# Optimization experiments

Measured on AMD Instinct MI355X. Metric: run time of the kernel, lower is better.

## Reference

```python
import jax, jax.numpy as jnp
import numpy as np


def setup_inputs() -> dict:
    key = jax.random.key(0)
    k1, k2, k3, k4 = jax.random.split(key, 4)
    L, d, n_tokens = 4096, 2048, 4096
    x = jax.random.normal(k1, (L, d), dtype=jnp.float32)
    Wq_w = jax.random.normal(k2, (d, d), dtype=jnp.float32) * (1.0 / np.sqrt(d))
    Pk = jax.random.normal(k3, (1, n_tokens, d), dtype=jnp.float32)
    Pv = jax.random.normal(k4, (1, n_tokens, d), dtype=jnp.float32)
    return {"x": x, "Wq_w": Wq_w, "Pk": Pk, "Pv": Pv, "sliding_window_size": 1024}


def reference(x, Wq_w, Pk, Pv, sliding_window_size):
    # x: (L, d); Pk/Pv: (1, n_tokens, d). Single-head cross attention to a
    # fixed parameter token bank with a bidirectional sliding-window mask
    # |q_idx - kv_idx| < sliding_window_size (flex_attention semantics,
    # default scale = 1/sqrt(d)).
    L, d = x.shape
    n_tokens = Pk.shape[1]
    scale = 1.0 / np.sqrt(d).astype(np.float32)

    q = x @ Wq_w.T                                    # (L, d)
    scores = jnp.einsum('ld,td->lt', q, Pk[0]) * scale  # (L, n_tokens)

    q_idx = jnp.arange(L)[:, None]
    kv_idx = jnp.arange(n_tokens)[None, :]
    mask = jnp.abs(q_idx - kv_idx) < sliding_window_size  # (L, n_tokens)

    neg_inf = jnp.asarray(jnp.finfo(scores.dtype).min, scores.dtype)
    probs = jax.nn.softmax(jnp.where(mask, scores, neg_inf), axis=-1)
    y = jnp.einsum('lt,td->ld', probs, Pv[0])         # (L, d)
    return y[None, :, :]                              # (1, L, d) after squeeze(1)
```

## Files before the change

### kernel.cpp

```cpp
#include <hip/hip_runtime.h>


using bf16x8 = __attribute__((ext_vector_type(8))) short;
using f32x4  = __attribute__((ext_vector_type(4))) float;

#define LDIM 4096
#define TDIM 4096
#define DDIM 2048

static __device__ __forceinline__ unsigned short f2bf(float f) {
  union { float f; unsigned u; } c; c.f = f;
  unsigned r = c.u + 0x7FFFu + ((c.u >> 16) & 1u);
  return (unsigned short)(r >> 16);
}
static __device__ __forceinline__ unsigned pack2(float a, float b) {
  return (unsigned)f2bf(a) | ((unsigned)f2bf(b) << 16);
}

static __device__ __forceinline__ void gload16(const void* g, void* l) {
  __builtin_amdgcn_global_load_lds((const __attribute__((address_space(1))) void*)g,
                                   (__attribute__((address_space(3))) void*)l, 16, 0, 0);
}

__global__ __launch_bounds__(256) void k_cvt(const float* __restrict__ in,
                                             unsigned short* __restrict__ out, int n8) {
  int i = blockIdx.x * 256 + threadIdx.x;
  if (i >= n8) return;
  const float4* p = (const float4*)(in + (size_t)i * 8);
  float4 a = p[0], b = p[1];
  uint4 o = { pack2(a.x, a.y), pack2(a.z, a.w), pack2(b.x, b.y), pack2(b.z, b.w) };
  *(uint4*)(out + (size_t)i * 8) = o;
}

__global__ __launch_bounds__(256) void k_trans(const float* __restrict__ V,
                                               unsigned short* __restrict__ Vt) {
  __shared__ unsigned short tile[64][65];
  const int t0 = blockIdx.x * 64;
  const int j0 = blockIdx.y * 64;
  const int tid = threadIdx.x;
  const int r = tid >> 4;
  const int c = (tid & 15) * 4;
#pragma unroll
  for (int rr = 0; rr < 64; rr += 16) {
    float4 v = *(const float4*)(V + (size_t)(t0 + r + rr) * DDIM + j0 + c);
    tile[r + rr][c + 0] = f2bf(v.x);
    tile[r + rr][c + 1] = f2bf(v.y);
    tile[r + rr][c + 2] = f2bf(v.z);
    tile[r + rr][c + 3] = f2bf(v.w);
  }
  __syncthreads();
#pragma unroll
  for (int rr = 0; rr < 64; rr += 16) {
    ushort4 o = { tile[c + 0][r + rr], tile[c + 1][r + rr],
                  tile[c + 2][r + rr], tile[c + 3][r + rr] };
    *(ushort4*)(Vt + (size_t)(j0 + r + rr) * TDIM + t0 + c) = o;
  }
}

static __device__ __forceinline__ void gemm_loop(const unsigned short* __restrict__ A,
                                                 const unsigned short* __restrict__ B,
                                                 int m0, int n0, long lda, long ldb,
                                                 int kbeg, int kend,
                                                 unsigned short* As, unsigned short* Bs,
                                                 f32x4 (&acc)[4][4]) {
  const int tid = threadIdx.x;
  const int wave = tid >> 6, lane = tid & 63;
  const int quad = lane >> 4, l16 = lane & 15;
  const int wm = wave >> 1, wn = wave & 1;
  const int srow = wave * 32 + (lane >> 2);
  const int scol = (lane & 3) * 8;

  for (int k0 = kbeg; k0 < kend; k0 += 32) {
    const unsigned short* gA = A + (long)(m0 + srow) * lda + k0 + scol;
    const unsigned short* gB = B + (long)(n0 + srow) * ldb + k0 + scol;
    gload16(gA,            As + wave * 1024);
    gload16(gA + 16 * lda, As + wave * 1024 + 512);
    gload16(gB,            Bs + wave * 1024);
    gload16(gB + 16 * ldb, Bs + wave * 1024 + 512);
    __syncthreads();
    bf16x8 af[4], bf[4];
#pragma unroll
    for (int i = 0; i < 4; i++)
      af[i] = *(const bf16x8*)&As[(wm * 64 + i * 16 + l16) * 32 + quad * 8];
#pragma unroll
    for (int i = 0; i < 4; i++)
      bf[i] = *(const bf16x8*)&Bs[(wn * 64 + i * 16 + l16) * 32 + quad * 8];
#pragma unroll
    for (int i = 0; i < 4; i++)
#pragma unroll
      for (int j = 0; j < 4; j++)
        acc[i][j] = __builtin_amdgcn_mfma_f32_16x16x32_bf16(af[i], bf[j], acc[i][j], 0, 0, 0);
    __syncthreads();
  }
}

__global__ __launch_bounds__(256) void k1_qgemm(const unsigned short* __restrict__ X,
                                                const unsigned short* __restrict__ W,
                                                unsigned short* __restrict__ q) {
  __shared__ __align__(16) unsigned short As[128 * 32];
  __shared__ __align__(16) unsigned short Bs[128 * 32];
  f32x4 acc[4][4] = {};
  const int m0 = blockIdx.y * 128, n0 = blockIdx.x * 128;
  gemm_loop(X, W, m0, n0, DDIM, DDIM, 0, DDIM, As, Bs, acc);
  const int tid = threadIdx.x;
  const int wave = tid >> 6, lane = tid & 63;
  const int quad = lane >> 4, l16 = lane & 15, wm = wave >> 1, wn = wave & 1;
#pragma unroll
  for (int i = 0; i < 4; i++)
#pragma unroll
    for (int j = 0; j < 4; j++)
#pragma unroll
      for (int r = 0; r < 4; r++) {
        int row = m0 + wm * 64 + i * 16 + quad * 4 + r;
        int col = n0 + wn * 64 + j * 16 + l16;
        q[(long)row * DDIM + col] = f2bf(acc[i][j][r]);
      }
}

__global__ __launch_bounds__(256) void k2_qk(const unsigned short* __restrict__ Q,
                                             const unsigned short* __restrict__ Kb,
                                             unsigned short* __restrict__ P,
                                             float* __restrict__ rowsum,
                                             const int* __restrict__ wptr) {
  const int w = *wptr;
  const int l0 = blockIdx.y * 128, t0 = blockIdx.x * 128;
  int lo = l0 - w + 1; if (lo < 0) lo = 0;
  int hi = l0 + 127 + w - 1; if (hi > TDIM - 1) hi = TDIM - 1;
  if ((int)blockIdx.x < (lo >> 7) || (int)blockIdx.x > (hi >> 7)) return;
  __shared__ __align__(16) unsigned short As[128 * 32];
  __shared__ __align__(16) unsigned short Bs[128 * 32];
  f32x4 acc[4][4] = {};
  gemm_loop(Q, Kb, l0, t0, DDIM, DDIM, 0, DDIM, As, Bs, acc);
  const float scale = 0.022097086912079608f;
  const int tid = threadIdx.x;
  const int wave = tid >> 6, lane = tid & 63;
  const int quad = lane >> 4, l16 = lane & 15, wm = wave >> 1, wn = wave & 1;
#pragma unroll
  for (int i = 0; i < 4; i++) {
    float rs[4] = {0.f, 0.f, 0.f, 0.f};
#pragma unroll
    for (int j = 0; j < 4; j++)
#pragma unroll
      for (int r = 0; r < 4; r++) {
        int l = l0 + wm * 64 + i * 16 + quad * 4 + r;
        int t = t0 + wn * 64 + j * 16 + l16;
        int dlt = l - t; dlt = dlt < 0 ? -dlt : dlt;
        float e = 0.f;
        if (dlt < w) e = __expf(acc[i][j][r] * scale);
        unsigned short bv = f2bf(e);
        P[(long)l * TDIM + t] = bv;
        rs[r] += __uint_as_float((unsigned)bv << 16);
      }
#pragma unroll
    for (int r = 0; r < 4; ++r) {
      float s = rs[r];
      s += __shfl_xor(s, 1);
      s += __shfl_xor(s, 2);
      s += __shfl_xor(s, 4);
      s += __shfl_xor(s, 8);
      if (l16 == 0) atomicAdd(&rowsum[l0 + wm * 64 + i * 16 + quad * 4 + r], s);
    }
  }
}

__global__ __launch_bounds__(256) void k3_pv(const unsigned short* __restrict__ P,
                                             const unsigned short* __restrict__ Vt,
                                             const float* __restrict__ rowsum,
                                             float* __restrict__ Y,
                                             const int* __restrict__ wptr) {
  const int w = *wptr;
  const int l0 = blockIdx.y * 128, j0 = blockIdx.x * 128;
  int lo = l0 - w + 1; if (lo < 0) lo = 0;
  int hi = l0 + 127 + w - 1; if (hi > TDIM - 1) hi = TDIM - 1;
  const int kb = (lo >> 7) * 128, ke = ((hi >> 7) + 1) * 128;
  __shared__ __align__(16) unsigned short As[128 * 32];
  __shared__ __align__(16) unsigned short Bs[128 * 32];
  f32x4 acc[4][4] = {};
  gemm_loop(P, Vt, l0, j0, TDIM, TDIM, kb, ke, As, Bs, acc);
  const int tid = threadIdx.x;
  const int wave = tid >> 6, lane = tid & 63;
  const int quad = lane >> 4, l16 = lane & 15, wm = wave >> 1, wn = wave & 1;
#pragma unroll
  for (int i = 0; i < 4; i++)
#pragma unroll
    for (int r = 0; r < 4; r++) {
      const int l = l0 + wm * 64 + i * 16 + quad * 4 + r;
      const float inv = 1.0f / rowsum[l];
#pragma unroll
      for (int j = 0; j < 4; j++)
        Y[(long)l * DDIM + j0 + wn * 64 + j * 16 + l16] = acc[i][j][r] * inv;
    }
}

extern "C" void kernel_launch(void* const* d_in, const int* in_sizes, int n_in,
                              void* d_out, int out_size, void* d_ws, size_t ws_size,
                              hipStream_t stream) {
  const float* x  = (const float*)d_in[0];
  const float* Wq = (const float*)d_in[1];
  const float* Pk = (const float*)d_in[2];
  const float* Pv = (const float*)d_in[3];
  const int* wptr = (const int*)d_in[4];
  float* Y = (float*)d_out;

  unsigned short* base = (unsigned short*)d_ws;
  unsigned short* Pm = base;
  unsigned short* xb = base;
  unsigned short* wb = base + (size_t)LDIM * DDIM;
  unsigned short* kb = base + (size_t)TDIM * TDIM;
  unsigned short* vt = kb + (size_t)TDIM * DDIM;
  unsigned short* qb = vt + (size_t)DDIM * TDIM;
  float* rowsum = (float*)(qb + (size_t)LDIM * DDIM);

  hipMemsetAsync(rowsum, 0, LDIM * sizeof(float), stream);
  k_cvt<<<LDIM * DDIM / 8 / 256, 256, 0, stream>>>(x, xb, LDIM * DDIM / 8);
  k_cvt<<<DDIM * DDIM / 8 / 256, 256, 0, stream>>>(Wq, wb, DDIM * DDIM / 8);
  k_cvt<<<TDIM * DDIM / 8 / 256, 256, 0, stream>>>(Pk, kb, TDIM * DDIM / 8);
  k_trans<<<dim3(TDIM / 64, DDIM / 64), 256, 0, stream>>>(Pv, vt);
  k1_qgemm<<<dim3(DDIM / 128, LDIM / 128), 256, 0, stream>>>(xb, wb, qb);
  k2_qk<<<dim3(TDIM / 128, LDIM / 128), 256, 0, stream>>>(qb, kb, Pm, rowsum, wptr);
  k3_pv<<<dim3(DDIM / 128, LDIM / 128), 256, 0, stream>>>(Pm, vt, rowsum, Y, wptr);
}
```

Measured before the change: 319.0 us.

## Fuse prep kernels and widen GEMM K-tile to 64 with XOR-swizzled LDS

Merges the three fp32-to-bf16 conversion launches, the V transpose and the rowsum memset into one prep kernel, removing several launches. The transpose now writes 16-byte vector stores. The shared GEMM loop moves from a K step of 32 to 64 and uses an XOR swizzle on LDS chunks, which halves the number of barriers per unit of K and is meant to cut LDS bank conflicts on fragment reads. This doubles the LDS footprint per block, which may reduce occupancy.

```diff
diff --git a/kernel.cpp b/kernel.cpp
--- a/kernel.cpp
+++ b/kernel.cpp
@@ -16,45 +16,55 @@
 static __device__ __forceinline__ unsigned pack2(float a, float b) {
   return (unsigned)f2bf(a) | ((unsigned)f2bf(b) << 16);
 }
-
 static __device__ __forceinline__ void gload16(const void* g, void* l) {
   __builtin_amdgcn_global_load_lds((const __attribute__((address_space(1))) void*)g,
                                    (__attribute__((address_space(3))) void*)l, 16, 0, 0);
 }
 
-__global__ __launch_bounds__(256) void k_cvt(const float* __restrict__ in,
-                                             unsigned short* __restrict__ out, int n8) {
-  int i = blockIdx.x * 256 + threadIdx.x;
-  if (i >= n8) return;
-  const float4* p = (const float4*)(in + (size_t)i * 8);
-  float4 a = p[0], b = p[1];
-  uint4 o = { pack2(a.x, a.y), pack2(a.z, a.w), pack2(b.x, b.y), pack2(b.z, b.w) };
-  *(uint4*)(out + (size_t)i * 8) = o;
-}
-
-__global__ __launch_bounds__(256) void k_trans(const float* __restrict__ V,
-                                               unsigned short* __restrict__ Vt) {
-  __shared__ unsigned short tile[64][65];
-  const int t0 = blockIdx.x * 64;
-  const int j0 = blockIdx.y * 64;
-  const int tid = threadIdx.x;
-  const int r = tid >> 4;
-  const int c = (tid & 15) * 4;
+__global__ __launch_bounds__(256) void k_prep(const float* __restrict__ x,
+                                              const float* __restrict__ Wq,
+                                              const float* __restrict__ Pk,
+                                              const float* __restrict__ Pv,
+                                              unsigned short* __restrict__ xb,
+                                              unsigned short* __restrict__ wb,
+                                              unsigned short* __restrict__ kb,
+                                              unsigned short* __restrict__ vt,
+                                              float* __restrict__ rowsum) {
+  const int tid = threadIdx.x;
+  const int b = blockIdx.x;
+  if (b < 10240) {
+    const float* in; unsigned short* out; size_t i;
+    if (b < 4096)      { in = x;  out = xb; i = (size_t)b * 256 + tid; }
+    else if (b < 6144) { in = Wq; out = wb; i = (size_t)(b - 4096) * 256 + tid; }
+    else               { in = Pk; out = kb; i = (size_t)(b - 6144) * 256 + tid; }
+    const float4* p = (const float4*)(in + i * 8);
+    float4 a = p[0], c = p[1];
+    uint4 o = { pack2(a.x, a.y), pack2(a.z, a.w), pack2(c.x, c.y), pack2(c.z, c.w) };
+    *(uint4*)(out + i * 8) = o;
+    return;
+  }
+  if (b == 12288) {
+    for (int k = tid; k < LDIM; k += 256) rowsum[k] = 0.f;
+    return;
+  }
+  __shared__ unsigned short tile[64][72];
+  const int b2 = b - 10240;
+  const int t0 = (b2 & 63) * 64, j0 = (b2 >> 6) * 64;
+  const int r = tid >> 4, c4 = (tid & 15) * 4;
 #pragma unroll
   for (int rr = 0; rr < 64; rr += 16) {
-    float4 v = *(const float4*)(V + (size_t)(t0 + r + rr) * DDIM + j0 + c);
-    tile[r + rr][c + 0] = f2bf(v.x);
-    tile[r + rr][c + 1] = f2bf(v.y);
-    tile[r + rr][c + 2] = f2bf(v.z);
-    tile[r + rr][c + 3] = f2bf(v.w);
+    float4 v = *(const float4*)(Pv + (size_t)(t0 + r + rr) * DDIM + j0 + c4);
+    tile[c4 + 0][r + rr] = f2bf(v.x);
+    tile[c4 + 1][r + rr] = f2bf(v.y);
+    tile[c4 + 2][r + rr] = f2bf(v.z);
+    tile[c4 + 3][r + rr] = f2bf(v.w);
   }
   __syncthreads();
-#pragma unroll
-  for (int rr = 0; rr < 64; rr += 16) {
-    ushort4 o = { tile[c + 0][r + rr], tile[c + 1][r + rr],
-                  tile[c + 2][r + rr], tile[c + 3][r + rr] };
-    *(ushort4*)(Vt + (size_t)(j0 + r + rr) * TDIM + t0 + c) = o;
-  }
+  const int jr = tid >> 3, tc = (tid & 7) * 8;
+#pragma unroll
+  for (int jj = 0; jj < 64; jj += 32)
+    *(uint4*)(vt + (size_t)(j0 + jr + jj) * TDIM + t0 + tc) =
+        *(const uint4*)&tile[jr + jj][tc];
 }
 
 static __device__ __forceinline__ void gemm_loop(const unsigned short* __restrict__ A,
@@ -67,29 +77,37 @@
   const int wave = tid >> 6, lane = tid & 63;
   const int quad = lane >> 4, l16 = lane & 15;
   const int wm = wave >> 1, wn = wave & 1;
-  const int srow = wave * 32 + (lane >> 2);
-  const int scol = (lane & 3) * 8;
-
-  for (int k0 = kbeg; k0 < kend; k0 += 32) {
-    const unsigned short* gA = A + (long)(m0 + srow) * lda + k0 + scol;
-    const unsigned short* gB = B + (long)(n0 + srow) * ldb + k0 + scol;
-    gload16(gA,            As + wave * 1024);
-    gload16(gA + 16 * lda, As + wave * 1024 + 512);
-    gload16(gB,            Bs + wave * 1024);
-    gload16(gB + 16 * ldb, Bs + wave * 1024 + 512);
+  const int srow = tid >> 3;
+  const int scb = (tid & 7) ^ (srow & 7);
+  const int fr = l16 & 7;
+
+  const unsigned short* gA = A + (long)(m0 + srow) * lda + scb * 8;
+  const unsigned short* gB = B + (long)(n0 + srow) * ldb + scb * 8;
+  unsigned short* lA = As + wave * 512;
+  unsigned short* lB = Bs + wave * 512;
+
+  for (int k0 = kbeg; k0 < kend; k0 += 64) {
+#pragma unroll
+    for (int c = 0; c < 4; c++) {
+      gload16(gA + (long)c * 32 * lda + k0, lA + c * 2048);
+      gload16(gB + (long)c * 32 * ldb + k0, lB + c * 2048);
+    }
     __syncthreads();
-    bf16x8 af[4], bf[4];
-#pragma unroll
-    for (int i = 0; i < 4; i++)
-      af[i] = *(const bf16x8*)&As[(wm * 64 + i * 16 + l16) * 32 + quad * 8];
-#pragma unroll
-    for (int i = 0; i < 4; i++)
-      bf[i] = *(const bf16x8*)&Bs[(wn * 64 + i * 16 + l16) * 32 + quad * 8];
-#pragma unroll
-    for (int i = 0; i < 4; i++)
+#pragma unroll
+    for (int s = 0; s < 2; s++) {
+      bf16x8 af[4], bfr[4];
+#pragma unroll
+      for (int i = 0; i < 4; i++)
+        af[i] = *(const bf16x8*)&As[((wm * 64 + i * 16 + l16) * 8 + ((s * 4 + quad) ^ fr)) * 8];
 #pragma unroll
       for (int j = 0; j < 4; j++)
-        acc[i][j] = __builtin_amdgcn_mfma_f32_16x16x32_bf16(af[i], bf[j], acc[i][j], 0, 0, 0);
+        bfr[j] = *(const bf16x8*)&Bs[((wn * 64 + j * 16 + l16) * 8 + ((s * 4 + quad) ^ fr)) * 8];
+#pragma unroll
+      for (int i = 0; i < 4; i++)
+#pragma unroll
+        for (int j = 0; j < 4; j++)
+          acc[i][j] = __builtin_amdgcn_mfma_f32_16x16x32_bf16(af[i], bfr[j], acc[i][j], 0, 0, 0);
+    }
     __syncthreads();
   }
 }
@@ -97,8 +115,8 @@
 __global__ __launch_bounds__(256) void k1_qgemm(const unsigned short* __restrict__ X,
                                                 const unsigned short* __restrict__ W,
                                                 unsigned short* __restrict__ q) {
-  __shared__ __align__(16) unsigned short As[128 * 32];
-  __shared__ __align__(16) unsigned short Bs[128 * 32];
+  __shared__ __align__(16) unsigned short As[128 * 64];
+  __shared__ __align__(16) unsigned short Bs[128 * 64];
   f32x4 acc[4][4] = {};
   const int m0 = blockIdx.y * 128, n0 = blockIdx.x * 128;
   gemm_loop(X, W, m0, n0, DDIM, DDIM, 0, DDIM, As, Bs, acc);
@@ -127,8 +145,8 @@
   int lo = l0 - w + 1; if (lo < 0) lo = 0;
   int hi = l0 + 127 + w - 1; if (hi > TDIM - 1) hi = TDIM - 1;
   if ((int)blockIdx.x < (lo >> 7) || (int)blockIdx.x > (hi >> 7)) return;
-  __shared__ __align__(16) unsigned short As[128 * 32];
-  __shared__ __align__(16) unsigned short Bs[128 * 32];
+  __shared__ __align__(16) unsigned short As[128 * 64];
+  __shared__ __align__(16) unsigned short Bs[128 * 64];
   f32x4 acc[4][4] = {};
   gemm_loop(Q, Kb, l0, t0, DDIM, DDIM, 0, DDIM, As, Bs, acc);
   const float scale = 0.022097086912079608f;
@@ -173,8 +191,8 @@
   int lo = l0 - w + 1; if (lo < 0) lo = 0;
   int hi = l0 + 127 + w - 1; if (hi > TDIM - 1) hi = TDIM - 1;
   const int kb = (lo >> 7) * 128, ke = ((hi >> 7) + 1) * 128;
-  __shared__ __align__(16) unsigned short As[128 * 32];
-  __shared__ __align__(16) unsigned short Bs[128 * 32];
+  __shared__ __align__(16) unsigned short As[128 * 64];
+  __shared__ __align__(16) unsigned short Bs[128 * 64];
   f32x4 acc[4][4] = {};
   gemm_loop(P, Vt, l0, j0, TDIM, TDIM, kb, ke, As, Bs, acc);
   const int tid = threadIdx.x;
@@ -211,11 +229,7 @@
   unsigned short* qb = vt + (size_t)DDIM * TDIM;
   float* rowsum = (float*)(qb + (size_t)LDIM * DDIM);
 
-  hipMemsetAsync(rowsum, 0, LDIM * sizeof(float), stream);
-  k_cvt<<<LDIM * DDIM / 8 / 256, 256, 0, stream>>>(x, xb, LDIM * DDIM / 8);
-  k_cvt<<<DDIM * DDIM / 8 / 256, 256, 0, stream>>>(Wq, wb, DDIM * DDIM / 8);
-  k_cvt<<<TDIM * DDIM / 8 / 256, 256, 0, stream>>>(Pk, kb, TDIM * DDIM / 8);
-  k_trans<<<dim3(TDIM / 64, DDIM / 64), 256, 0, stream>>>(Pv, vt);
+  k_prep<<<12289, 256, 0, stream>>>(x, Wq, Pk, Pv, xb, wb, kb, vt, rowsum);
   k1_qgemm<<<dim3(DDIM / 128, LDIM / 128), 256, 0, stream>>>(xb, wb, qb);
   k2_qk<<<dim3(TDIM / 128, LDIM / 128), 256, 0, stream>>>(qb, kb, Pm, rowsum, wptr);
   k3_pv<<<dim3(DDIM / 128, LDIM / 128), 256, 0, stream>>>(Pm, vt, rowsum, Y, wptr);
```

Result: faster. 310.5 us (-2.7%).
